# Kernel tuning notes

Measured on AMD Instinct MI355X. Metric: run time of the kernel, lower is better.

## Reference

```python
import jax, jax.numpy as jnp
import numpy as np

D_IN = 3072      # == d_out (code reshapes x directly into heads)
D_OUT = 3072
N_HEADS = 16
HEAD_DIM = D_OUT // N_HEADS          # 192
D_C = D_OUT // 3                     # 1024, compressed latent dim
LN_EPS = 1e-5


def setup_inputs() -> dict:
    key = jax.random.key(0)
    ks = jax.random.split(key, 8)
    s = 0.02
    return {
        "x": jax.random.normal(ks[0], (2, 2048, D_IN), dtype=jnp.float32),
        "W_query": jax.random.normal(ks[1], (D_OUT, D_IN), dtype=jnp.float32) * s,
        "W_kv": jax.random.normal(ks[2], (D_C, D_IN), dtype=jnp.float32) * s,
        "W_uk": jax.random.normal(ks[3], (D_OUT, D_C), dtype=jnp.float32) * s,
        "W_uv": jax.random.normal(ks[4], (D_OUT, D_C), dtype=jnp.float32) * s,
        "W_out": jax.random.normal(ks[5], (D_OUT, D_OUT), dtype=jnp.float32) * s,
        "b_out": jnp.zeros((D_OUT,), dtype=jnp.float32),
        "ln_g": jnp.ones((D_C,), dtype=jnp.float32),
        "ln_b": jnp.zeros((D_C,), dtype=jnp.float32),
    }


def reference(x, W_query, W_kv, W_uk, W_uv, W_out, b_out, ln_g, ln_b):
    B, T, D = x.shape
    past_length = 0  # prefill, kv_cache=None

    # absorbed K projection: (d_out, d_in) @ (d_out, d_c) -> (H, head_dim, d_c)
    absorbed_k = (W_query @ W_uk).reshape(N_HEADS, HEAD_DIM, D_C)

    # compressed latent c_kv = LayerNorm(x @ W_kv^T), shape (B, S, d_c)
    c = x @ W_kv.T
    mu = jnp.mean(c, axis=-1, keepdims=True)
    var = jnp.mean(jnp.square(c - mu), axis=-1, keepdims=True)
    c_kv = (c - mu) * jax.lax.rsqrt(var + LN_EPS) * ln_g + ln_b
    S = c_kv.shape[1]

    # values decompressed: (B, S, H, head_dim)
    v = (c_kv @ W_uv.T).reshape(B, S, N_HEADS, HEAD_DIM)

    # queries: raw x reshaped into heads (as in the original code)
    q = x.reshape(B, T, N_HEADS, HEAD_DIM)

    # scores in compressed space: q @ absorbed_k @ c_kv^T
    tmp = jnp.einsum("bthd,hdc->bhtc", q, absorbed_k)           # (B,H,T,d_c)
    scores = jnp.einsum("bhtc,bsc->bhts", tmp, c_kv)
    scores = scores / np.float32(np.sqrt(HEAD_DIM))

    # causal mask with past_length offset (tril diagonal=past_length)
    row = jnp.arange(T)[:, None]
    col = jnp.arange(S)[None, :]
    mask = col <= (row + past_length)                            # (T,S) bool
    scores = jnp.where(mask[None, None], scores, -jnp.inf)

    weights = jax.nn.softmax(scores, axis=-1)                    # (B,H,T,S)

    ctx = jnp.einsum("bhts,bshd->bthd", weights, v).reshape(B, T, D_OUT)
    out = ctx @ W_out.T + b_out
    return out, c_kv
```

## Files before the change

### kernel.cpp

```cpp
#include <hip/hip_runtime.h>
#include <hip/hip_bf16.h>
#include <math.h>

#define BB 2
#define TT 2048
#define DD 3072
#define NH 16
#define HD 192
#define DC 1024

typedef __attribute__((ext_vector_type(8))) short bh8;
typedef __attribute__((ext_vector_type(4))) float f32x4;
typedef unsigned int u32;

__device__ __forceinline__ short f2b(float f) {
  __hip_bfloat16 h = __float2bfloat16(f);
  return *reinterpret_cast<short*>(&h);
}

__device__ __forceinline__ void gload16(const void* g, void* lds) {
  __builtin_amdgcn_global_load_lds(
      (const __attribute__((address_space(1))) u32*)g,
      (__attribute__((address_space(3))) u32*)lds, 16, 0, 0);
}

__global__ __launch_bounds__(256) void cast_f2b_k(const float* __restrict__ in,
                                                  short* __restrict__ out) {
  size_t i = ((size_t)blockIdx.x * 256 + threadIdx.x) * 8;
  float4 v0 = *(const float4*)&in[i];
  float4 v1 = *(const float4*)&in[i + 4];
  bh8 o;
  o[0] = f2b(v0.x); o[1] = f2b(v0.y); o[2] = f2b(v0.z); o[3] = f2b(v0.w);
  o[4] = f2b(v1.x); o[5] = f2b(v1.y); o[6] = f2b(v1.z); o[7] = f2b(v1.w);
  *(bh8*)&out[i] = o;
}

__global__ __launch_bounds__(256) void castT_f2b_k(const float* __restrict__ in,
                                                   short* __restrict__ out,
                                                   int R, int C) {
  __shared__ float t[64][65];
  const int cx = blockIdx.x * 64, ry = blockIdx.y * 64;
  const int tid = threadIdx.x, lx = tid & 15, ly = tid >> 4;
#pragma unroll
  for (int i = 0; i < 4; ++i) {
    int r = ly + i * 16;
    float4 v = *(const float4*)&in[(size_t)(ry + r) * C + cx + lx * 4];
    t[r][lx * 4 + 0] = v.x; t[r][lx * 4 + 1] = v.y;
    t[r][lx * 4 + 2] = v.z; t[r][lx * 4 + 3] = v.w;
  }
  __syncthreads();
#pragma unroll
  for (int i = 0; i < 4; ++i) {
    int c = ly + i * 16;
    ushort4 v;
    v.x = (unsigned short)f2b(t[lx * 4 + 0][c]);
    v.y = (unsigned short)f2b(t[lx * 4 + 1][c]);
    v.z = (unsigned short)f2b(t[lx * 4 + 2][c]);
    v.w = (unsigned short)f2b(t[lx * 4 + 3][c]);
    *(ushort4*)&out[(size_t)(cx + c) * R + ry + lx * 4] = v;
  }
}

__global__ __launch_bounds__(256) void transpose_b16_k(
    const unsigned short* __restrict__ in, unsigned short* __restrict__ out,
    int ldin) {
  __shared__ unsigned short t[64][65];
  const unsigned short* ib = in + (size_t)blockIdx.z * TT * ldin;
  unsigned short* ob = out + (size_t)blockIdx.z * DD * TT;
  const int cx = blockIdx.x * 64, ry = blockIdx.y * 64;
  const int tid = threadIdx.x, lx = tid & 15, ly = tid >> 4;
#pragma unroll
  for (int i = 0; i < 4; ++i) {
    int r = ly + i * 16;
    ushort4 v = *(const ushort4*)&ib[(size_t)(ry + r) * ldin + cx + lx * 4];
    t[r][lx * 4 + 0] = v.x; t[r][lx * 4 + 1] = v.y;
    t[r][lx * 4 + 2] = v.z; t[r][lx * 4 + 3] = v.w;
  }
  __syncthreads();
#pragma unroll
  for (int i = 0; i < 4; ++i) {
    int c = ly + i * 16;
    ushort4 v;
    v.x = t[lx * 4 + 0][c]; v.y = t[lx * 4 + 1][c];
    v.z = t[lx * 4 + 2][c]; v.w = t[lx * 4 + 3][c];
    *(ushort4*)&ob[(size_t)(cx + c) * TT + ry + lx * 4] = v;
  }
}

template <bool OUTBF, bool BIAS>
__global__ __launch_bounds__(256) void gemm_bf16(
    const short* __restrict__ A, const short* __restrict__ Bt,
    const float* __restrict__ bias, void* __restrict__ Cout,
    int M, int N, int Klen, int lda, int ldb, size_t zoff_bytes) {
  __shared__ short As[4096];
  __shared__ short Bs[4096];
  const int tid = threadIdx.x;
  const int w = tid >> 6, l = tid & 63, lm = l & 15, lg = l >> 4;
  const int wr = w >> 1, wc = w & 1;

  const int bz = blockIdx.z;
  A += (size_t)bz * Klen;
  Bt += (size_t)bz * Klen;
  Cout = (void*)((char*)Cout + (size_t)bz * zoff_bytes);

  const int nwg = gridDim.x * gridDim.y;
  const int flat = blockIdx.y * gridDim.x + blockIdx.x;
  const int wgid = (flat & 7) * (nwg >> 3) + (flat >> 3);
  const int m0 = (wgid / gridDim.x) * 128, n0 = (wgid % gridDim.x) * 128;

  f32x4 acc[4][4] = {};

  for (int k0 = 0; k0 < Klen; k0 += 32) {
    __syncthreads();
#pragma unroll
    for (int c = 0; c < 2; ++c) {
      int p = c * 256 + w * 64 + l;
      int row = p >> 2, kc = p & 3;
      int g = kc ^ ((row >> 1) & 3);
      gload16(&A[(size_t)(m0 + row) * lda + k0 + g * 8],
              &As[(c * 256 + w * 64) * 8]);
      gload16(&Bt[(size_t)(n0 + row) * ldb + k0 + g * 8],
              &Bs[(c * 256 + w * 64) * 8]);
    }
    __syncthreads();

    bh8 a[4], b[4];
#pragma unroll
    for (int mi = 0; mi < 4; ++mi) {
      int r = wr * 64 + mi * 16 + lm;
      a[mi] = *(const bh8*)&As[r * 32 + ((lg ^ ((r >> 1) & 3)) << 3)];
    }
#pragma unroll
    for (int ni = 0; ni < 4; ++ni) {
      int r = wc * 64 + ni * 16 + lm;
      b[ni] = *(const bh8*)&Bs[r * 32 + ((lg ^ ((r >> 1) & 3)) << 3)];
    }
#pragma unroll
    for (int mi = 0; mi < 4; ++mi)
#pragma unroll
      for (int ni = 0; ni < 4; ++ni)
        acc[mi][ni] = __builtin_amdgcn_mfma_f32_16x16x32_bf16(
            a[mi], b[ni], acc[mi][ni], 0, 0, 0);
  }

#pragma unroll
  for (int mi = 0; mi < 4; ++mi) {
#pragma unroll
    for (int ni = 0; ni < 4; ++ni) {
      int row = m0 + wr * 64 + mi * 16 + lg * 4;
      int col = n0 + wc * 64 + ni * 16 + lm;
      float bi = 0.f;
      if (BIAS) bi = bias[col];
#pragma unroll
      for (int r = 0; r < 4; ++r) {
        float v = acc[mi][ni][r] + bi;
        if (OUTBF)
          ((short*)Cout)[(size_t)(row + r) * N + col] = f2b(v);
        else
          ((float*)Cout)[(size_t)(row + r) * N + col] = v;
      }
    }
  }
}

__global__ __launch_bounds__(256) void ln_k(const float* __restrict__ cp0,
                                            const float* __restrict__ cp1,
                                            const float* __restrict__ g,
                                            const float* __restrict__ bta,
                                            float* __restrict__ o32,
                                            short* __restrict__ o16) {
  const int row = blockIdx.x;
  const int tid = threadIdx.x;
  __shared__ float red1[4];
  __shared__ float red2[4];

  float4 va = *(const float4*)&cp0[(size_t)row * DC + tid * 4];
  float4 vb = *(const float4*)&cp1[(size_t)row * DC + tid * 4];
  float4 v;
  v.x = va.x + vb.x; v.y = va.y + vb.y; v.z = va.z + vb.z; v.w = va.w + vb.w;
  float s = v.x + v.y + v.z + v.w;
#pragma unroll
  for (int mk = 32; mk; mk >>= 1) s += __shfl_xor(s, mk, 64);
  if ((tid & 63) == 0) red1[tid >> 6] = s;
  __syncthreads();
  float mu = (red1[0] + red1[1] + red1[2] + red1[3]) * (1.f / DC);

  float dx = v.x - mu, dy = v.y - mu, dz = v.z - mu, dw = v.w - mu;
  float s2 = dx * dx + dy * dy + dz * dz + dw * dw;
#pragma unroll
  for (int mk = 32; mk; mk >>= 1) s2 += __shfl_xor(s2, mk, 64);
  if ((tid & 63) == 0) red2[tid >> 6] = s2;
  __syncthreads();
  float var = (red2[0] + red2[1] + red2[2] + red2[3]) * (1.f / DC);
  float rs = rsqrtf(var + 1e-5f);

  float4 gg = *(const float4*)&g[tid * 4];
  float4 bb = *(const float4*)&bta[tid * 4];
  float4 o;
  o.x = dx * rs * gg.x + bb.x;
  o.y = dy * rs * gg.y + bb.y;
  o.z = dz * rs * gg.z + bb.z;
  o.w = dw * rs * gg.w + bb.w;
  *(float4*)&o32[(size_t)row * DC + tid * 4] = o;
  ushort4 ob;
  ob.x = (unsigned short)f2b(o.x); ob.y = (unsigned short)f2b(o.y);
  ob.z = (unsigned short)f2b(o.z); ob.w = (unsigned short)f2b(o.w);
  *(ushort4*)&o16[(size_t)row * DC + tid * 4] = ob;
}

__global__ __launch_bounds__(256) void attn_mfma(
    const short* __restrict__ xb, const short* __restrict__ kf,
    const short* __restrict__ vT, short* __restrict__ ctx) {
  __shared__ short Ks[64 * 192];
  __shared__ short Vs[192 * 64];
  __shared__ short Ps[4][16 * 64];

  const int idx = blockIdx.x;
  const int qt = 31 - (idx >> 5);
  const int bh = idx & 31;
  const int h = bh & 15, b = bh >> 4;
  const int tid = threadIdx.x, w = tid >> 6, l = tid & 63;
  const int lm = l & 15, lg = l >> 4;
  const int qw0 = qt * 64 + w * 16;
  const float QS = 0.07216878364870323f;

  bh8 qf[6];
  {
    const short* qrow = &xb[(size_t)(b * TT + qw0 + lm) * DD + h * HD];
#pragma unroll
    for (int kq = 0; kq < 6; ++kq)
      qf[kq] = *(const bh8*)&qrow[kq * 32 + lg * 8];
  }

  f32x4 o[12] = {};
  float mrun[4], lrun[4];
#pragma unroll
  for (int r = 0; r < 4; ++r) { mrun[r] = -INFINITY; lrun[r] = 0.f; }

  for (int st = 0; st <= qt; ++st) {
    const int s0 = st * 64;
    __syncthreads();
#pragma unroll
    for (int c = 0; c < 6; ++c) {
      int p = c * 256 + w * 64 + l;
      {
        int krow = p / 24, kc = p - krow * 24;
        int g = kc ^ (krow & 7);
        gload16(&kf[(size_t)(b * TT + s0 + krow) * DD + h * HD + g * 8],
                &Ks[(c * 256 + w * 64) * 8]);
      }
      {
        int vrow = p >> 3, vc = p & 7;
        int gv = vc ^ (vrow & 7);
        gload16(&vT[(size_t)((b * NH + h) * HD + vrow) * TT + s0 + gv * 8],
                &Vs[(c * 256 + w * 64) * 8]);
      }
    }
    __syncthreads();

    f32x4 s[4] = {};
    __builtin_amdgcn_s_setprio(1);
#pragma unroll
    for (int nf = 0; nf < 4; ++nf) {
      const int krow = nf * 16 + lm;
      const short* kr = &Ks[krow * 192];
#pragma unroll
      for (int kq = 0; kq < 6; ++kq) {
        bh8 kb = *(const bh8*)&kr[(((kq * 4 + lg) ^ (krow & 7)) << 3)];
        s[nf] = __builtin_amdgcn_mfma_f32_16x16x32_bf16(qf[kq], kb, s[nf],
                                                        0, 0, 0);
      }
    }
    __builtin_amdgcn_s_setprio(0);

    float pv[4][4];
#pragma unroll
    for (int nf = 0; nf < 4; ++nf)
#pragma unroll
      for (int r = 0; r < 4; ++r) pv[nf][r] = s[nf][r] * QS;
    if (st == qt) {
#pragma unroll
      for (int nf = 0; nf < 4; ++nf)
#pragma unroll
        for (int r = 0; r < 4; ++r)
          if (nf * 16 + lm > w * 16 + lg * 4 + r) pv[nf][r] = -INFINITY;
    }
#pragma unroll
    for (int r = 0; r < 4; ++r) {
      float mt = fmaxf(fmaxf(pv[0][r], pv[1][r]), fmaxf(pv[2][r], pv[3][r]));
#pragma unroll
      for (int mk = 1; mk < 16; mk <<= 1) mt = fmaxf(mt, __shfl_xor(mt, mk));
      float mnew = fmaxf(mrun[r], mt);
      float corr = __expf(mrun[r] - mnew);
      mrun[r] = mnew;
      float ls = 0.f;
#pragma unroll
      for (int nf = 0; nf < 4; ++nf) {
        float p = __expf(pv[nf][r] - mnew);
        pv[nf][r] = p;
        ls += p;
      }
#pragma unroll
      for (int mk = 1; mk < 16; mk <<= 1) ls += __shfl_xor(ls, mk);
      lrun[r] = lrun[r] * corr + ls;
#pragma unroll
      for (int nf = 0; nf < 12; ++nf) o[nf][r] *= corr;
    }
#pragma unroll
    for (int nf = 0; nf < 4; ++nf)
#pragma unroll
      for (int r = 0; r < 4; ++r) {
        int prow = lg * 4 + r;
        int col = nf * 16 + lm;
        int sc = (((col >> 3) ^ (prow & 7)) << 3) + (col & 7);
        Ps[w][prow * 64 + sc] = f2b(pv[nf][r]);
      }

    bh8 pa0, pa1;
    {
      int prow = lm;
      pa0 = *(const bh8*)&Ps[w][prow * 64 + ((lg ^ (prow & 7)) << 3)];
      pa1 = *(const bh8*)&Ps[w][prow * 64 + (((4 + lg) ^ (prow & 7)) << 3)];
    }
    __builtin_amdgcn_s_setprio(1);
#pragma unroll
    for (int nf = 0; nf < 12; ++nf) {
      int drow = nf * 16 + lm;
      const short* vr = &Vs[drow * 64];
      bh8 vb0 = *(const bh8*)&vr[((lg ^ (drow & 7)) << 3)];
      bh8 vb1 = *(const bh8*)&vr[(((4 + lg) ^ (drow & 7)) << 3)];
      o[nf] = __builtin_amdgcn_mfma_f32_16x16x32_bf16(pa0, vb0, o[nf], 0, 0, 0);
      o[nf] = __builtin_amdgcn_mfma_f32_16x16x32_bf16(pa1, vb1, o[nf], 0, 0, 0);
    }
    __builtin_amdgcn_s_setprio(0);
  }

#pragma unroll
  for (int r = 0; r < 4; ++r) {
    float inv = 1.f / lrun[r];
    int row = qw0 + lg * 4 + r;
    short* cp = &ctx[(size_t)(b * TT + row) * DD + h * HD];
#pragma unroll
    for (int nf = 0; nf < 12; ++nf)
      cp[nf * 16 + lm] = f2b(o[nf][r] * inv);
  }
}

extern "C" void kernel_launch(void* const* d_in, const int* in_sizes, int n_in,
                              void* d_out, int out_size, void* d_ws,
                              size_t ws_size, hipStream_t stream) {
  const float* x    = (const float*)d_in[0];
  const float* Wq   = (const float*)d_in[1];
  const float* Wkv  = (const float*)d_in[2];
  const float* Wuk  = (const float*)d_in[3];
  const float* Wuv  = (const float*)d_in[4];
  const float* Wout = (const float*)d_in[5];
  const float* bout = (const float*)d_in[6];
  const float* lng  = (const float*)d_in[7];
  const float* lnb  = (const float*)d_in[8];

  float* out   = (float*)d_out;
  float* ckv32 = out + (size_t)BB * TT * DD;

  char* W = (char*)d_ws;
  short* xb     = (short*)(W);
  short* wbuf   = (short*)(W + 25165824);
  short* wukT   = (short*)(W + 44040192);
  short* wkvb   = (short*)(W + 50331648);
  short* wuvb   = (short*)(W + 56623104);
  short* akb    = (short*)(W + 62914560);
  float* cpre0  = (float*)(W + 69206016);
  short* ckvb   = (short*)(W + 85983232);
  short* kfullb = (short*)(W + 94371840);
  short* vfullb = (short*)(W + 119537664);
  float* cpre1  = (float*)(W + 144703488);
  short* vTb    = (short*)(W + 144703488);
  short* ctxb   = vfullb;
  const size_t G2_ZOFF = (size_t)(144703488 - 69206016);

  cast_f2b_k<<<6144, 256, 0, stream>>>(x, xb);
  cast_f2b_k<<<4608, 256, 0, stream>>>(Wq, wbuf);
  cast_f2b_k<<<1536, 256, 0, stream>>>(Wkv, wkvb);
  cast_f2b_k<<<1536, 256, 0, stream>>>(Wuv, wuvb);
  castT_f2b_k<<<dim3(16, 48), 256, 0, stream>>>(Wuk, wukT, 3072, 1024);

  gemm_bf16<true, false><<<dim3(8, 24), 256, 0, stream>>>(
      wbuf, wukT, nullptr, akb, 3072, 1024, 3072, 3072, 3072, 0);
  cast_f2b_k<<<4608, 256, 0, stream>>>(Wout, wbuf);
  gemm_bf16<false, false><<<dim3(8, 32, 2), 256, 0, stream>>>(
      xb, wkvb, nullptr, cpre0, 4096, 1024, 1536, 3072, 3072, G2_ZOFF);
  ln_k<<<4096, 256, 0, stream>>>(cpre0, cpre1, lng, lnb, ckv32, ckvb);
  gemm_bf16<true, false><<<dim3(24, 32), 256, 0, stream>>>(
      ckvb, akb, nullptr, kfullb, 4096, 3072, 1024, 1024, 1024, 0);
  gemm_bf16<true, false><<<dim3(24, 32), 256, 0, stream>>>(
      ckvb, wuvb, nullptr, vfullb, 4096, 3072, 1024, 1024, 1024, 0);
  transpose_b16_k<<<dim3(48, 32, 2), 256, 0, stream>>>(
      (const unsigned short*)vfullb, (unsigned short*)vTb, DD);
  attn_mfma<<<1024, 256, 0, stream>>>(xb, kfullb, vTb, ctxb);
  gemm_bf16<false, true><<<dim3(24, 32), 256, 0, stream>>>(
      ctxb, wbuf, bout, out, 4096, 3072, 3072, 3072, 3072, 0);
}
```

Baseline: 469.1 us.

## Widen GEMM K-tile, fuse V transpose into GEMM epilogue, split-K absorbed-K GEMM

The bf16 GEMM now stages 64-wide K tiles in LDS with an 8-way XOR swizzle, doing two MFMA sub-steps per barrier pair. This halves the number of synchronisations per K. The V up-projection GEMM gains an epilogue mode that writes the transposed layout directly, so the separate transpose kernel and its round trip to memory go away. The W_query·W_uk GEMM (only 192 blocks) is split along K into two z-slices with fp32 partials, then reduced and cast by a new sum_cast kernel to fill more CUs. In exchange, LDS per block doubles, which may lower occupancy, and the transposed stores are 8-byte strided writes.

```diff
diff --git a/kernel.cpp b/kernel.cpp
--- a/kernel.cpp
+++ b/kernel.cpp
@@ -35,6 +35,22 @@
   *(bh8*)&out[i] = o;
 }
 
+__global__ __launch_bounds__(256) void sum_cast_k(const float* __restrict__ p0,
+                                                  const float* __restrict__ p1,
+                                                  short* __restrict__ out) {
+  size_t i = ((size_t)blockIdx.x * 256 + threadIdx.x) * 8;
+  float4 a0 = *(const float4*)&p0[i];
+  float4 a1 = *(const float4*)&p0[i + 4];
+  float4 b0 = *(const float4*)&p1[i];
+  float4 b1 = *(const float4*)&p1[i + 4];
+  bh8 o;
+  o[0] = f2b(a0.x + b0.x); o[1] = f2b(a0.y + b0.y);
+  o[2] = f2b(a0.z + b0.z); o[3] = f2b(a0.w + b0.w);
+  o[4] = f2b(a1.x + b1.x); o[5] = f2b(a1.y + b1.y);
+  o[6] = f2b(a1.z + b1.z); o[7] = f2b(a1.w + b1.w);
+  *(bh8*)&out[i] = o;
+}
+
 __global__ __launch_bounds__(256) void castT_f2b_k(const float* __restrict__ in,
                                                    short* __restrict__ out,
                                                    int R, int C) {
@@ -61,39 +77,13 @@
   }
 }
 
-__global__ __launch_bounds__(256) void transpose_b16_k(
-    const unsigned short* __restrict__ in, unsigned short* __restrict__ out,
-    int ldin) {
-  __shared__ unsigned short t[64][65];
-  const unsigned short* ib = in + (size_t)blockIdx.z * TT * ldin;
-  unsigned short* ob = out + (size_t)blockIdx.z * DD * TT;
-  const int cx = blockIdx.x * 64, ry = blockIdx.y * 64;
-  const int tid = threadIdx.x, lx = tid & 15, ly = tid >> 4;
-#pragma unroll
-  for (int i = 0; i < 4; ++i) {
-    int r = ly + i * 16;
-    ushort4 v = *(const ushort4*)&ib[(size_t)(ry + r) * ldin + cx + lx * 4];
-    t[r][lx * 4 + 0] = v.x; t[r][lx * 4 + 1] = v.y;
-    t[r][lx * 4 + 2] = v.z; t[r][lx * 4 + 3] = v.w;
-  }
-  __syncthreads();
-#pragma unroll
-  for (int i = 0; i < 4; ++i) {
-    int c = ly + i * 16;
-    ushort4 v;
-    v.x = t[lx * 4 + 0][c]; v.y = t[lx * 4 + 1][c];
-    v.z = t[lx * 4 + 2][c]; v.w = t[lx * 4 + 3][c];
-    *(ushort4*)&ob[(size_t)(cx + c) * TT + ry + lx * 4] = v;
-  }
-}
-
-template <bool OUTBF, bool BIAS>
+template <int OUTMODE, bool BIAS>
 __global__ __launch_bounds__(256) void gemm_bf16(
     const short* __restrict__ A, const short* __restrict__ Bt,
     const float* __restrict__ bias, void* __restrict__ Cout,
     int M, int N, int Klen, int lda, int ldb, size_t zoff_bytes) {
-  __shared__ short As[4096];
-  __shared__ short Bs[4096];
+  __shared__ short As[8192];
+  __shared__ short Bs[8192];
   const int tid = threadIdx.x;
   const int w = tid >> 6, l = tid & 63, lm = l & 15, lg = l >> 4;
   const int wr = w >> 1, wc = w & 1;
@@ -110,13 +100,13 @@
 
   f32x4 acc[4][4] = {};
 
-  for (int k0 = 0; k0 < Klen; k0 += 32) {
+  for (int k0 = 0; k0 < Klen; k0 += 64) {
     __syncthreads();
 #pragma unroll
-    for (int c = 0; c < 2; ++c) {
+    for (int c = 0; c < 4; ++c) {
       int p = c * 256 + w * 64 + l;
-      int row = p >> 2, kc = p & 3;
-      int g = kc ^ ((row >> 1) & 3);
+      int row = p >> 3, kc = p & 7;
+      int g = kc ^ (row & 7);
       gload16(&A[(size_t)(m0 + row) * lda + k0 + g * 8],
               &As[(c * 256 + w * 64) * 8]);
       gload16(&Bt[(size_t)(n0 + row) * ldb + k0 + g * 8],
@@ -124,23 +114,26 @@
     }
     __syncthreads();
 
-    bh8 a[4], b[4];
-#pragma unroll
-    for (int mi = 0; mi < 4; ++mi) {
-      int r = wr * 64 + mi * 16 + lm;
-      a[mi] = *(const bh8*)&As[r * 32 + ((lg ^ ((r >> 1) & 3)) << 3)];
-    }
-#pragma unroll
-    for (int ni = 0; ni < 4; ++ni) {
-      int r = wc * 64 + ni * 16 + lm;
-      b[ni] = *(const bh8*)&Bs[r * 32 + ((lg ^ ((r >> 1) & 3)) << 3)];
-    }
-#pragma unroll
-    for (int mi = 0; mi < 4; ++mi)
-#pragma unroll
-      for (int ni = 0; ni < 4; ++ni)
-        acc[mi][ni] = __builtin_amdgcn_mfma_f32_16x16x32_bf16(
-            a[mi], b[ni], acc[mi][ni], 0, 0, 0);
+#pragma unroll
+    for (int kh = 0; kh < 2; ++kh) {
+      bh8 a[4], b[4];
+#pragma unroll
+      for (int mi = 0; mi < 4; ++mi) {
+        int r = wr * 64 + mi * 16 + lm;
+        a[mi] = *(const bh8*)&As[r * 64 + (((kh * 4 + lg) ^ (r & 7)) << 3)];
+      }
+#pragma unroll
+      for (int ni = 0; ni < 4; ++ni) {
+        int r = wc * 64 + ni * 16 + lm;
+        b[ni] = *(const bh8*)&Bs[r * 64 + (((kh * 4 + lg) ^ (r & 7)) << 3)];
+      }
+#pragma unroll
+      for (int mi = 0; mi < 4; ++mi)
+#pragma unroll
+        for (int ni = 0; ni < 4; ++ni)
+          acc[mi][ni] = __builtin_amdgcn_mfma_f32_16x16x32_bf16(
+              a[mi], b[ni], acc[mi][ni], 0, 0, 0);
+    }
   }
 
 #pragma unroll
@@ -151,13 +144,23 @@
       int col = n0 + wc * 64 + ni * 16 + lm;
       float bi = 0.f;
       if (BIAS) bi = bias[col];
-#pragma unroll
-      for (int r = 0; r < 4; ++r) {
-        float v = acc[mi][ni][r] + bi;
-        if (OUTBF)
-          ((short*)Cout)[(size_t)(row + r) * N + col] = f2b(v);
-        else
-          ((float*)Cout)[(size_t)(row + r) * N + col] = v;
+      if (OUTMODE == 2) {
+        int b = row >> 11, t = row & 2047;
+        ushort4 o;
+        o.x = (unsigned short)f2b(acc[mi][ni][0]);
+        o.y = (unsigned short)f2b(acc[mi][ni][1]);
+        o.z = (unsigned short)f2b(acc[mi][ni][2]);
+        o.w = (unsigned short)f2b(acc[mi][ni][3]);
+        *(ushort4*)&((short*)Cout)[((size_t)(b * DD + col)) * TT + t] = o;
+      } else {
+#pragma unroll
+        for (int r = 0; r < 4; ++r) {
+          float v = acc[mi][ni][r] + bi;
+          if (OUTMODE == 1)
+            ((short*)Cout)[(size_t)(row + r) * N + col] = f2b(v);
+          else
+            ((float*)Cout)[(size_t)(row + r) * N + col] = v;
+        }
       }
     }
   }
@@ -372,10 +375,12 @@
   float* cpre0  = (float*)(W + 69206016);
   short* ckvb   = (short*)(W + 85983232);
   short* kfullb = (short*)(W + 94371840);
-  short* vfullb = (short*)(W + 119537664);
+  float* g1p0   = (float*)(W + 94371840);
+  short* ctxb   = (short*)(W + 119537664);
+  float* g1p1   = (float*)(W + 119537664);
   float* cpre1  = (float*)(W + 144703488);
   short* vTb    = (short*)(W + 144703488);
-  short* ctxb   = vfullb;
+  const size_t G1_ZOFF = (size_t)(119537664 - 94371840);
   const size_t G2_ZOFF = (size_t)(144703488 - 69206016);
 
   cast_f2b_k<<<6144, 256, 0, stream>>>(x, xb);
@@ -384,19 +389,18 @@
   cast_f2b_k<<<1536, 256, 0, stream>>>(Wuv, wuvb);
   castT_f2b_k<<<dim3(16, 48), 256, 0, stream>>>(Wuk, wukT, 3072, 1024);
 
-  gemm_bf16<true, false><<<dim3(8, 24), 256, 0, stream>>>(
-      wbuf, wukT, nullptr, akb, 3072, 1024, 3072, 3072, 3072, 0);
+  gemm_bf16<0, false><<<dim3(8, 24, 2), 256, 0, stream>>>(
+      wbuf, wukT, nullptr, g1p0, 3072, 1024, 1536, 3072, 3072, G1_ZOFF);
+  sum_cast_k<<<1536, 256, 0, stream>>>(g1p0, g1p1, akb);
   cast_f2b_k<<<4608, 256, 0, stream>>>(Wout, wbuf);
-  gemm_bf16<false, false><<<dim3(8, 32, 2), 256, 0, stream>>>(
+  gemm_bf16<0, false><<<dim3(8, 32, 2), 256, 0, stream>>>(
       xb, wkvb, nullptr, cpre0, 4096, 1024, 1536, 3072, 3072, G2_ZOFF);
   ln_k<<<4096, 256, 0, stream>>>(cpre0, cpre1, lng, lnb, ckv32, ckvb);
-  gemm_bf16<true, false><<<dim3(24, 32), 256, 0, stream>>>(
+  gemm_bf16<1, false><<<dim3(24, 32), 256, 0, stream>>>(
       ckvb, akb, nullptr, kfullb, 4096, 3072, 1024, 1024, 1024, 0);
-  gemm_bf16<true, false><<<dim3(24, 32), 256, 0, stream>>>(
-      ckvb, wuvb, nullptr, vfullb, 4096, 3072, 1024, 1024, 1024, 0);
-  transpose_b16_k<<<dim3(48, 32, 2), 256, 0, stream>>>(
-      (const unsigned short*)vfullb, (unsigned short*)vTb, DD);
+  gemm_bf16<2, false><<<dim3(24, 32), 256, 0, stream>>>(
+      ckvb, wuvb, nullptr, vTb, 4096, 3072, 1024, 1024, 1024, 0);
   attn_mfma<<<1024, 256, 0, stream>>>(xb, kfullb, vTb, ctxb);
-  gemm_bf16<false, true><<<dim3(24, 32), 256, 0, stream>>>(
+  gemm_bf16<0, true><<<dim3(24, 32), 256, 0, stream>>>(
       ctxb, wbuf, bout, out, 4096, 3072, 3072, 3072, 3072, 0);
 }
```

New measurement: 399.8 us. 1.17x faster.
